# Performance work log

Hardware: AMD Instinct MI355X
Metric: run time of the kernel (lower is better)

Reference implementation:

```python
import jax, jax.numpy as jnp
import numpy as np

B, T, V, D, H, E, K = 512, 80, 80, 128, 256, 8, 2
G1, G2 = 512, 256
EPS = 1e-5


def setup_inputs() -> dict:
    key = jax.random.key(0)
    ks = jax.random.split(key, 16)
    s = 0.05
    x = jax.random.randint(ks[0], (B, T), 0, V)
    emb = jax.random.normal(ks[1], (E, V, D), jnp.float32) * s
    Wih0 = jax.random.normal(ks[2], (E, 4 * H, D), jnp.float32) * s
    Whh0 = jax.random.normal(ks[3], (E, 4 * H, H), jnp.float32) * s
    bih0 = jnp.zeros((E, 4 * H), jnp.float32)
    bhh0 = jnp.zeros((E, 4 * H), jnp.float32)
    Wih1 = jax.random.normal(ks[4], (E, 4 * H, H), jnp.float32) * s
    Whh1 = jax.random.normal(ks[5], (E, 4 * H, H), jnp.float32) * s
    bih1 = jnp.zeros((E, 4 * H), jnp.float32)
    bhh1 = jnp.zeros((E, 4 * H), jnp.float32)
    fcw = jax.random.normal(ks[6], (E, V, H), jnp.float32) * s
    fcb = jnp.zeros((E, V), jnp.float32)
    gw1 = jax.random.normal(ks[7], (G1, D), jnp.float32) * s
    gb1 = jnp.zeros((G1,), jnp.float32)
    bn1_g = jnp.ones((G1,), jnp.float32)
    bn1_b = jnp.zeros((G1,), jnp.float32)
    bn1_m = jnp.zeros((G1,), jnp.float32)
    bn1_v = jnp.ones((G1,), jnp.float32)
    gw2 = jax.random.normal(ks[8], (G2, G1), jnp.float32) * s
    gb2 = jnp.zeros((G2,), jnp.float32)
    bn2_g = jnp.ones((G2,), jnp.float32)
    bn2_b = jnp.zeros((G2,), jnp.float32)
    bn2_m = jnp.zeros((G2,), jnp.float32)
    bn2_v = jnp.ones((G2,), jnp.float32)
    gw3 = jax.random.normal(ks[9], (E, G2), jnp.float32) * s
    gb3 = jnp.zeros((E,), jnp.float32)
    return dict(x=x, emb=emb, Wih0=Wih0, Whh0=Whh0, bih0=bih0, bhh0=bhh0,
                Wih1=Wih1, Whh1=Whh1, bih1=bih1, bhh1=bhh1, fcw=fcw, fcb=fcb,
                gw1=gw1, gb1=gb1, bn1_g=bn1_g, bn1_b=bn1_b, bn1_m=bn1_m, bn1_v=bn1_v,
                gw2=gw2, gb2=gb2, bn2_g=bn2_g, bn2_b=bn2_b, bn2_m=bn2_m, bn2_v=bn2_v,
                gw3=gw3, gb3=gb3)


def _lstm_layer(Wih, Whh, bih, bhh, xs):
    # xs: [B, T, Din] -> (hidden seq [B, T, H], final hidden [B, H]); torch gate order i,f,g,o
    h0 = jnp.zeros((xs.shape[0], Whh.shape[1]), xs.dtype)

    def step(carry, xt):
        h, c = carry
        z = xt @ Wih.T + bih + h @ Whh.T + bhh
        i, f, g, o = jnp.split(z, 4, axis=-1)
        c = jax.nn.sigmoid(f) * c + jax.nn.sigmoid(i) * jnp.tanh(g)
        h = jax.nn.sigmoid(o) * jnp.tanh(c)
        return (h, c), h

    (h, _), hs = jax.lax.scan(step, (h0, h0), jnp.swapaxes(xs, 0, 1))
    return jnp.swapaxes(hs, 0, 1), h


def _expert(emb_e, Wih0, Whh0, bih0, bhh0, Wih1, Whh1, bih1, bhh1, fcw, fcb, x):
    e = emb_e[x]                                   # [B, T, D]
    hs1, _ = _lstm_layer(Wih0, Whh0, bih0, bhh0, e)
    _, h2 = _lstm_layer(Wih1, Whh1, bih1, bhh1, hs1)
    return h2 @ fcw.T + fcb                        # [B, V] (fc on last timestep)


def _bn_eval(x, g, b, m, v):
    return (x - m) * jax.lax.rsqrt(v + EPS) * g + b


def _forward(x, emb, Wih0, Whh0, bih0, bhh0, Wih1, Whh1, bih1, bhh1, fcw, fcb,
             gw1, gb1, bn1_g, bn1_b, bn1_m, bn1_v,
             gw2, gb2, bn2_g, bn2_b, bn2_m, bn2_v, gw3, gb3):
    # gating features: expert 0 embedding, mean over time  [B, D]
    feat = emb[0][x].mean(axis=1)
    h = jax.nn.relu(_bn_eval(feat @ gw1.T + gb1, bn1_g, bn1_b, bn1_m, bn1_v))
    h = jax.nn.relu(_bn_eval(h @ gw2.T + gb2, bn2_g, bn2_b, bn2_m, bn2_v))
    logits = h @ gw3.T + gb3                       # [B, E]  (eval: no noise)
    scores = jax.nn.softmax(logits, axis=-1)
    tv, ti = jax.lax.top_k(scores, K)              # [B, K]
    w = tv / tv.sum(axis=-1, keepdims=True)
    # per-expert combine weight (top-k indices are distinct, at most one slot per expert)
    we = (w[..., None] * jax.nn.one_hot(ti, E, dtype=w.dtype)).sum(axis=1)  # [B, E]
    eouts = jax.vmap(_expert, in_axes=(0,) * 11 + (None,))(
        emb, Wih0, Whh0, bih0, bhh0, Wih1, Whh1, bih1, bhh1, fcw, fcb, x)   # [E, B, V]
    return jnp.einsum('ebc,be->bc', eouts, we)


def reference(x, emb, Wih0, Whh0, bih0, bhh0, Wih1, Whh1, bih1, bhh1, fcw, fcb,
              gw1, gb1, bn1_g, bn1_b, bn1_m, bn1_v,
              gw2, gb2, bn2_g, bn2_b, bn2_m, bn2_v, gw3, gb3):
    return _forward(x, emb, Wih0, Whh0, bih0, bhh0, Wih1, Whh1, bih1, bhh1, fcw, fcb,
                    gw1, gb1, bn1_g, bn1_b, bn1_m, bn1_v,
                    gw2, gb2, bn2_g, bn2_b, bn2_m, bn2_v, gw3, gb3)
```

## Files before the change

kernel.cpp:

```cpp
#include <hip/hip_runtime.h>
#include <hip/hip_bf16.h>
#include <math.h>

#define BB 512
#define TT 80
#define VV 80
#define DD 128
#define HH 256
#define FH 1024
#define EE 8
#define GG1 512
#define GG2 256
#define MT 16
#define NT 72
#define SLOTS (NT*MT)
#define CCK 16

typedef __attribute__((ext_vector_type(8))) short bf16x8;
typedef __attribute__((ext_vector_type(4))) float f32x4;
typedef __attribute__((ext_vector_type(4))) unsigned int u32x4;

__device__ __forceinline__ float bf2f(unsigned short u) {
    unsigned int v = ((unsigned int)u) << 16;
    return __builtin_bit_cast(float, v);
}
__device__ __forceinline__ unsigned short f2bf(float f) {
    __hip_bfloat16 h = __float2bfloat16(f);
    return __builtin_bit_cast(unsigned short, h);
}
__device__ __forceinline__ float sigm(float x) { return 1.f / (1.f + __expf(-x)); }
__device__ __forceinline__ float tanh_f(float x) {
    float ax = fabsf(x);
    float r = 1.f - 2.f / (__expf(2.f * ax) + 1.f);
    return x < 0.f ? -r : r;
}

__global__ void prep_kernel(const float* __restrict__ Whh0, const float* __restrict__ Wih1,
                            const float* __restrict__ Whh1,
                            const float* __restrict__ bih1, const float* __restrict__ bhh1,
                            unsigned short* __restrict__ WR0, unsigned short* __restrict__ WR1,
                            unsigned short* __restrict__ WG, float* __restrict__ bsum1)
{
    const int NB = 262144;
    const int ntot = 3 * NB + EE * FH;
    for (int idx = blockIdx.x * blockDim.x + threadIdx.x; idx < ntot;
         idx += gridDim.x * blockDim.x) {
        if (idx < 3 * NB) {
            int arr = idx / NB;
            int p = idx - arr * NB;
            int gc, kk, e;
            const float* src;
            if (arr < 2) {
                int l = p & 63, nf = (p >> 6) & 7, kb = (p >> 9) & 7, w = (p >> 12) & 7;
                e = (p >> 15) & 7;
                int g = nf >> 1, hc = nf & 1;
                gc = g * 256 + w * 32 + hc * 16 + (l & 15);
                kk = kb * 32 + ((l >> 4) * 8);
                src = (arr == 0) ? Whh0 : Whh1;
            } else {
                int l = p & 63, kb = (p >> 6) & 7, gf = (p >> 9) & 63; e = (p >> 15) & 7;
                gc = gf * 16 + (l & 15);
                kk = kb * 32 + ((l >> 4) * 8);
                src = Wih1;
            }
            const float* sp = src + ((size_t)e * FH + gc) * HH + kk;
            float4 f0 = *(const float4*)sp;
            float4 f1 = *(const float4*)(sp + 4);
            unsigned short out[8];
            out[0] = f2bf(f0.x); out[1] = f2bf(f0.y); out[2] = f2bf(f0.z); out[3] = f2bf(f0.w);
            out[4] = f2bf(f1.x); out[5] = f2bf(f1.y); out[6] = f2bf(f1.z); out[7] = f2bf(f1.w);
            unsigned short* dst = (arr == 0 ? WR0 : arr == 1 ? WR1 : WG) + (size_t)p * 8;
            *(uint4*)dst = *(uint4*)out;
        } else {
            int p = idx - 3 * NB;
            bsum1[p] = bih1[p] + bhh1[p];
        }
    }
}

__global__ __launch_bounds__(256)
void embw_kernel(const float* __restrict__ emb, const float* __restrict__ Wih0,
                 const float* __restrict__ bih0, const float* __restrict__ bhh0,
                 unsigned short* __restrict__ embT)
{
    const int e = blockIdx.x, g = blockIdx.y;
    const int tid = threadIdx.x;
    const int gc = g * 256 + tid;
    __shared__ float er[DD * VV];
    for (int i = tid; i < VV * DD; i += 256) {
        int tok = i >> 7, d = i & 127;
        er[d * VV + tok] = emb[((size_t)e * VV + tok) * DD + d];
    }
    __syncthreads();
    float acc[VV];
    #pragma unroll
    for (int v = 0; v < VV; v++) acc[v] = 0.f;
    const float* wr = Wih0 + ((size_t)e * FH + gc) * DD;
    for (int d = 0; d < DD; d++) {
        float wv = wr[d];
        #pragma unroll
        for (int v4 = 0; v4 < VV; v4 += 4) {
            float4 ev = *(const float4*)&er[d * VV + v4];
            acc[v4] += ev.x * wv; acc[v4 + 1] += ev.y * wv;
            acc[v4 + 2] += ev.z * wv; acc[v4 + 3] += ev.w * wv;
        }
    }
    float bias = bih0[e * FH + gc] + bhh0[e * FH + gc];
    #pragma unroll 4
    for (int v = 0; v < VV; v++)
        embT[(((size_t)e * VV + v) * 256 + tid) * 4 + g] = f2bf(acc[v] + bias);
}

__global__ __launch_bounds__(128)
void gating_kernel(const int* __restrict__ x, const float* __restrict__ emb,
                   const float* __restrict__ gw1, const float* __restrict__ gb1,
                   const float* __restrict__ g1g, const float* __restrict__ g1b,
                   const float* __restrict__ g1m, const float* __restrict__ g1v,
                   const float* __restrict__ gw2, const float* __restrict__ gb2,
                   const float* __restrict__ g2g, const float* __restrict__ g2b,
                   const float* __restrict__ g2m, const float* __restrict__ g2v,
                   const float* __restrict__ gw3, const float* __restrict__ gb3,
                   int* __restrict__ route_i, float* __restrict__ route_w)
{
    int b = blockIdx.x, tid = threadIdx.x;
    __shared__ int tk[TT];
    __shared__ float feat[DD];
    __shared__ float h1[GG1];
    __shared__ float h2[GG2];
    __shared__ float lg[EE];
    if (tid < TT) tk[tid] = x[b * TT + tid];
    __syncthreads();
    if (tid < DD) {
        float s = 0.f;
        for (int t = 0; t < TT; t++) s += emb[(size_t)tk[t] * DD + tid];
        feat[tid] = s * (1.f / TT);
    }
    __syncthreads();
    for (int j = tid; j < GG1; j += 128) {
        float s = gb1[j];
        const float* wr = gw1 + (size_t)j * DD;
        for (int d = 0; d < DD; d++) s += feat[d] * wr[d];
        float y = (s - g1m[j]) / sqrtf(g1v[j] + 1e-5f) * g1g[j] + g1b[j];
        h1[j] = y > 0.f ? y : 0.f;
    }
    __syncthreads();
    for (int j = tid; j < GG2; j += 128) {
        float s = gb2[j];
        const float* wr = gw2 + (size_t)j * GG1;
        for (int d = 0; d < GG1; d++) s += h1[d] * wr[d];
        float y = (s - g2m[j]) / sqrtf(g2v[j] + 1e-5f) * g2g[j] + g2b[j];
        h2[j] = y > 0.f ? y : 0.f;
    }
    __syncthreads();
    if (tid < EE) {
        float s = gb3[tid];
        const float* wr = gw3 + (size_t)tid * GG2;
        for (int d = 0; d < GG2; d++) s += h2[d] * wr[d];
        lg[tid] = s;
    }
    __syncthreads();
    if (tid == 0) {
        int i0 = 0;
        for (int i = 1; i < EE; i++) if (lg[i] > lg[i0]) i0 = i;
        int i1 = (i0 == 0) ? 1 : 0;
        for (int i = 0; i < EE; i++) if (i != i0 && lg[i] > lg[i1]) i1 = i;
        float e1 = expf(lg[i1] - lg[i0]);
        float inv = 1.f / (1.f + e1);
        route_i[b * 2] = i0; route_i[b * 2 + 1] = i1;
        route_w[b * 2] = inv; route_w[b * 2 + 1] = e1 * inv;
    }
}

__global__ __launch_bounds__(1024)
void route_kernel(const int* __restrict__ route_i, const float* __restrict__ route_w,
                  int* __restrict__ slot_b, int* __restrict__ slot_k,
                  float* __restrict__ slot_w, int* __restrict__ slot_e)
{
    __shared__ int wcnt[16][EE];
    __shared__ int cnt[EE];
    __shared__ int off[EE + 1];
    int tid = threadIdx.x;
    int lane = tid & 63, wv = tid >> 6;
    int e = route_i[tid];
    unsigned long long below = (1ull << lane) - 1ull;
    int rankw = 0;
    #pragma unroll
    for (int q = 0; q < EE; q++) {
        unsigned long long m = __ballot(e == q);
        if (q == e) rankw = __popcll(m & below);
        if (lane == 0) wcnt[wv][q] = __popcll(m);
    }
    __syncthreads();
    if (tid < EE) {
        int c = 0;
        for (int w2 = 0; w2 < 16; w2++) c += wcnt[w2][tid];
        cnt[tid] = c;
    }
    __syncthreads();
    if (tid == 0) {
        off[0] = 0;
        for (int q = 0; q < EE; q++) off[q + 1] = off[q] + ((cnt[q] + MT - 1) / MT) * MT;
    }
    __syncthreads();
    for (int s = tid; s < SLOTS; s += 1024) {
        int e2 = 0;
        if (s < off[EE]) { for (int q = 0; q < EE; q++) if (s >= off[q]) e2 = q; }
        slot_b[s] = -1; slot_k[s] = 0; slot_w[s] = 0.f; slot_e[s] = e2;
    }
    __syncthreads();
    int rank = rankw;
    for (int w2 = 0; w2 < wv; w2++) rank += wcnt[w2][e];
    int s = off[e] + rank;
    slot_b[s] = tid >> 1; slot_k[s] = tid & 1; slot_w[s] = route_w[tid];
}

template<int LAYER>
__device__ __forceinline__ void lstm_body(
    int t0, int tcount,
    const unsigned short* __restrict__ WR,
    const unsigned short* __restrict__ embT,
    const unsigned short* __restrict__ zin1,
    const int* __restrict__ x,
    const int* __restrict__ slot_b, const int* __restrict__ slot_e,
    unsigned short* __restrict__ h0seq, float* __restrict__ h1f,
    float* __restrict__ cst, unsigned short* __restrict__ hsv,
    unsigned short (*wlds)[8][8][512], unsigned short (*hbuf)[4096], int* toks)
{
    const int tile = blockIdx.x;
    if (slot_b[tile * MT] < 0) return;
    const int tid = threadIdx.x;
    const int lane = tid & 63;
    const int w = tid >> 6;
    const int e = slot_e[tile * MT];
    const int l15 = lane & 15;
    const int q = lane >> 4;
    const int col0 = w * 32 + l15;
    const int col1 = col0 + 16;
    const int sc0 = (((col0 >> 5) * 64 + 16 * ((col0 >> 3) & 3)) << 3) + (col0 & 7);
    const int sc1 = (((col1 >> 5) * 64 + 16 * ((col1 >> 3) & 3)) << 3) + (col1 & 7);

    const unsigned short* WBg = WR + ((size_t)(e * 8 + w) * 64) * 512 + (size_t)lane * 8;

    u32x4 wres[32];
    #pragma unroll
    for (int i = 0; i < 32; i++) wres[i] = *(const u32x4*)(WBg + (size_t)i * 512);
    #pragma unroll
    for (int i = 0; i < 32; i++) asm volatile("" : "+v"(wres[i]));

    #pragma unroll
    for (int i = 0; i < 16; i++)
        *(uint4*)&wlds[i >> 3][w][i & 7][lane * 8] = *(const uint4*)(WBg + (size_t)(32 + i) * 512);

    if (LAYER == 0) {
        for (int i = tid; i < tcount * 16; i += 512)
            toks[i] = x[max(slot_b[tile * MT + (i & 15)], 0) * TT + t0 + (i >> 4)];
    }

    if (t0 == 0) {
        *(f32x4*)&hbuf[0][tid * 8] = (f32x4){0.f, 0.f, 0.f, 0.f};
    } else {
        *(bf16x8*)&hbuf[0][tid * 8] = *(const bf16x8*)(hsv + (size_t)tile * 4096 + tid * 8);
    }
    float c[8];
    if (t0 == 0) {
        #pragma unroll
        for (int i = 0; i < 8; i++) c[i] = 0.f;
    } else {
        f32x4 v0 = *(const f32x4*)&cst[((size_t)(tile * 512 + tid)) * 8];
        f32x4 v1 = *(const f32x4*)&cst[((size_t)(tile * 512 + tid)) * 8 + 4];
        c[0]=v0[0]; c[1]=v0[1]; c[2]=v0[2]; c[3]=v0[3];
        c[4]=v1[0]; c[5]=v1[1]; c[6]=v1[2]; c[7]=v1[3];
    }

    __syncthreads();

    int cur = 0;
    for (int t = 0; t < tcount; t++) {
        const int nxt = cur ^ 1;

        u32x4 ws[8];
        #pragma unroll
        for (int nf = 0; nf < 8; nf++) ws[nf] = *(const u32x4*)(WBg + (size_t)(48 + nf) * 512);

        ushort4 za[4], zb[4];
        if (LAYER == 0) {
            #pragma unroll
            for (int reg = 0; reg < 4; reg++) {
                int tok = toks[t * 16 + q * 4 + reg];
                const unsigned short* zp = embT + ((size_t)(e * VV + tok)) * 1024;
                za[reg] = *(const ushort4*)(zp + col0 * 4);
                zb[reg] = *(const ushort4*)(zp + col1 * 4);
            }
        } else {
            const unsigned short* zp = zin1 + ((size_t)(tile * tcount + t)) * 16384;
            #pragma unroll
            for (int g = 0; g < 4; g++) {
                int gfa = g * 16 + w * 2;
                za[g] = *(const ushort4*)(zp + (gfa * 64 + lane) * 4);
                zb[g] = *(const ushort4*)(zp + ((gfa + 1) * 64 + lane) * 4);
            }
        }

        f32x4 acc[8];
        if (LAYER == 0) {
            #pragma unroll
            for (int reg = 0; reg < 4; reg++) {
                acc[0][reg] = bf2f(za[reg].x); acc[2][reg] = bf2f(za[reg].y);
                acc[4][reg] = bf2f(za[reg].z); acc[6][reg] = bf2f(za[reg].w);
                acc[1][reg] = bf2f(zb[reg].x); acc[3][reg] = bf2f(zb[reg].y);
                acc[5][reg] = bf2f(zb[reg].z); acc[7][reg] = bf2f(zb[reg].w);
            }
        } else {
            #pragma unroll
            for (int g = 0; g < 4; g++) {
                acc[g * 2][0] = bf2f(za[g].x); acc[g * 2][1] = bf2f(za[g].y);
                acc[g * 2][2] = bf2f(za[g].z); acc[g * 2][3] = bf2f(za[g].w);
                acc[g * 2 + 1][0] = bf2f(zb[g].x); acc[g * 2 + 1][1] = bf2f(zb[g].y);
                acc[g * 2 + 1][2] = bf2f(zb[g].z); acc[g * 2 + 1][3] = bf2f(zb[g].w);
            }
        }

        #pragma unroll
        for (int kb = 0; kb < 4; kb++) {
            bf16x8 a = *(const bf16x8*)&hbuf[cur][(kb * 64 + lane) * 8];
            #pragma unroll
            for (int nf = 0; nf < 8; nf++)
                acc[nf] = __builtin_amdgcn_mfma_f32_16x16x32_bf16(
                    a, __builtin_bit_cast(bf16x8, wres[kb * 8 + nf]), acc[nf], 0, 0, 0);
        }

        #pragma unroll
        for (int kbi = 0; kbi < 2; kbi++) {
            bf16x8 a = *(const bf16x8*)&hbuf[cur][((4 + kbi) * 64 + lane) * 8];
            #pragma unroll
            for (int nf = 0; nf < 8; nf++) {
                bf16x8 wl = *(const bf16x8*)&wlds[kbi][w][nf][lane * 8];
                acc[nf] = __builtin_amdgcn_mfma_f32_16x16x32_bf16(a, wl, acc[nf], 0, 0, 0);
            }
        }

        {
            bf16x8 a = *(const bf16x8*)&hbuf[cur][(6 * 64 + lane) * 8];
            #pragma unroll
            for (int nf = 0; nf < 8; nf++)
                acc[nf] = __builtin_amdgcn_mfma_f32_16x16x32_bf16(
                    a, __builtin_bit_cast(bf16x8, ws[nf]), acc[nf], 0, 0, 0);
        }
        #pragma unroll
        for (int nf = 0; nf < 8; nf++) ws[nf] = *(const u32x4*)(WBg + (size_t)(56 + nf) * 512);
        {
            bf16x8 a = *(const bf16x8*)&hbuf[cur][(7 * 64 + lane) * 8];
            #pragma unroll
            for (int nf = 0; nf < 8; nf++)
                acc[nf] = __builtin_amdgcn_mfma_f32_16x16x32_bf16(
                    a, __builtin_bit_cast(bf16x8, ws[nf]), acc[nf], 0, 0, 0);
        }

        #pragma unroll
        for (int reg = 0; reg < 4; reg++) {
            int r = q * 4 + reg;
            {
                float iv = acc[0][reg], fv = acc[2][reg], gv = acc[4][reg], ov = acc[6][reg];
                float cn = sigm(fv) * c[reg * 2] + sigm(iv) * tanh_f(gv);
                float hn = sigm(ov) * tanh_f(cn);
                c[reg * 2] = cn;
                hbuf[nxt][sc0 + r * 8] = f2bf(hn);
                if (LAYER == 1 && t0 + t == TT - 1)
                    h1f[((size_t)(tile * MT + r)) * HH + col0] = hn;
            }
            {
                float iv = acc[1][reg], fv = acc[3][reg], gv = acc[5][reg], ov = acc[7][reg];
                float cn = sigm(fv) * c[reg * 2 + 1] + sigm(iv) * tanh_f(gv);
                float hn = sigm(ov) * tanh_f(cn);
                c[reg * 2 + 1] = cn;
                hbuf[nxt][sc1 + r * 8] = f2bf(hn);
                if (LAYER == 1 && t0 + t == TT - 1)
                    h1f[((size_t)(tile * MT + r)) * HH + col1] = hn;
            }
        }
        __syncthreads();
        cur = nxt;
        if (LAYER == 0) {
            *(uint4*)(h0seq + ((size_t)(tile * tcount + t)) * 4096 + tid * 8) =
                *(const uint4*)&hbuf[cur][tid * 8];
        }
    }

    f32x4 v0, v1;
    v0[0]=c[0]; v0[1]=c[1]; v0[2]=c[2]; v0[3]=c[3];
    v1[0]=c[4]; v1[1]=c[5]; v1[2]=c[6]; v1[3]=c[7];
    *(f32x4*)&cst[((size_t)(tile * 512 + tid)) * 8] = v0;
    *(f32x4*)&cst[((size_t)(tile * 512 + tid)) * 8 + 4] = v1;
    *(uint4*)(hsv + (size_t)tile * 4096 + tid * 8) = *(const uint4*)&hbuf[cur][tid * 8];
}

__global__ __launch_bounds__(512, 1)
void lstm_fused(int t0_0, int t0_1, int tcount,
                const unsigned short* __restrict__ WR0, const unsigned short* __restrict__ WR1,
                const unsigned short* __restrict__ embT, const unsigned short* __restrict__ zin1,
                const int* __restrict__ x,
                const int* __restrict__ slot_b, const int* __restrict__ slot_e,
                unsigned short* __restrict__ h0seq, float* __restrict__ h1f,
                float* __restrict__ cst0, float* __restrict__ cst1,
                unsigned short* __restrict__ hsv0, unsigned short* __restrict__ hsv1)
{
    __shared__ unsigned short wlds[2][8][8][512];
    __shared__ unsigned short hbuf[2][4096];
    __shared__ int toks[CCK * 16];
    if (blockIdx.y == 0) {
        if (t0_0 < 0) return;
        lstm_body<0>(t0_0, tcount, WR0, embT, zin1, x, slot_b, slot_e,
                     h0seq, h1f, cst0, hsv0, wlds, hbuf, toks);
    } else {
        if (t0_1 < 0) return;
        lstm_body<1>(t0_1, tcount, WR1, embT, zin1, x, slot_b, slot_e,
                     h0seq, h1f, cst1, hsv1, wlds, hbuf, toks);
    }
}

__global__ __launch_bounds__(256)
void gemm_zin(int tcount,
              const unsigned short* __restrict__ h0seq,
              const unsigned short* __restrict__ WG,
              const float* __restrict__ bsum1,
              const int* __restrict__ slot_b, const int* __restrict__ slot_e,
              unsigned short* __restrict__ zin1)
{
    const int tile = blockIdx.x;
    if (slot_b[tile * MT] < 0) return;
    const int tch = blockIdx.y, nch = blockIdx.z;
    const int tid = threadIdx.x, lane = tid & 63, w = tid >> 6;
    const int e = slot_e[tile * MT];
    __shared__ unsigned short Abuf[32768];
    const unsigned short* Asrc = h0seq + ((size_t)(tile * tcount + tch * 8)) * 4096;
    #pragma unroll
    for (int i = 0; i < 16; i++) {
        int o = (i * 256 + tid) * 8;
        *(bf16x8*)&Abuf[o] = *(const bf16x8*)&Asrc[o];
    }
    __syncthreads();
    const unsigned short* Bp = WG + ((size_t)(e * 64 + nch * 16 + w * 4)) * 4096 + lane * 8;
    f32x4 acc[8][4];
    #pragma unroll
    for (int mf = 0; mf < 8; mf++)
        #pragma unroll
        for (int nfi = 0; nfi < 4; nfi++) acc[mf][nfi] = (f32x4){0.f, 0.f, 0.f, 0.f};
    #pragma unroll
    for (int kb = 0; kb < 8; kb++) {
        bf16x8 b0 = *(const bf16x8*)(Bp + 0 * 4096 + kb * 512);
        bf16x8 b1 = *(const bf16x8*)(Bp + 1 * 4096 + kb * 512);
        bf16x8 b2 = *(const bf16x8*)(Bp + 2 * 4096 + kb * 512);
        bf16x8 b3 = *(const bf16x8*)(Bp + 3 * 4096 + kb * 512);
        #pragma unroll
        for (int mf = 0; mf < 8; mf++) {
            bf16x8 a = *(const bf16x8*)&Abuf[(mf * 8 + kb) * 512 + lane * 8];
            acc[mf][0] = __builtin_amdgcn_mfma_f32_16x16x32_bf16(a, b0, acc[mf][0], 0, 0, 0);
            acc[mf][1] = __builtin_amdgcn_mfma_f32_16x16x32_bf16(a, b1, acc[mf][1], 0, 0, 0);
            acc[mf][2] = __builtin_amdgcn_mfma_f32_16x16x32_bf16(a, b2, acc[mf][2], 0, 0, 0);
            acc[mf][3] = __builtin_amdgcn_mfma_f32_16x16x32_bf16(a, b3, acc[mf][3], 0, 0, 0);
        }
    }
    const int l15 = lane & 15;
    #pragma unroll
    for (int mf = 0; mf < 8; mf++) {
        unsigned short* ob = zin1 + ((size_t)(tile * tcount + tch * 8 + mf)) * 16384;
        #pragma unroll
        for (int nfi = 0; nfi < 4; nfi++) {
            int gf = nch * 16 + w * 4 + nfi;
            float bs = bsum1[e * FH + gf * 16 + l15];
            ushort4 v;
            v.x = f2bf(acc[mf][nfi][0] + bs);
            v.y = f2bf(acc[mf][nfi][1] + bs);
            v.z = f2bf(acc[mf][nfi][2] + bs);
            v.w = f2bf(acc[mf][nfi][3] + bs);
            *(ushort4*)(ob + (size_t)(gf * 64 + lane) * 4) = v;
        }
    }
}

__global__ __launch_bounds__(256)
void fc_kernel(const float* __restrict__ fcw, const float* __restrict__ fcb,
               const float* __restrict__ h1f,
               const int* __restrict__ slot_b, const int* __restrict__ slot_k,
               const float* __restrict__ slot_w, const int* __restrict__ slot_e,
               float* __restrict__ wout)
{
    int s = blockIdx.x;
    int b = slot_b[s];
    if (b < 0) return;
    int tid = threadIdx.x;
    __shared__ float hv[HH];
    if (tid < HH) hv[tid] = h1f[(size_t)s * HH + tid];
    __syncthreads();
    int e = slot_e[s], kk = slot_k[s];
    float w = slot_w[s];
    for (int v = tid; v < VV; v += 256) {
        float sacc = fcb[e * VV + v];
        const float* fr = fcw + ((size_t)e * VV + v) * HH;
        #pragma unroll 4
        for (int d = 0; d < HH; d++) sacc += hv[d] * fr[d];
        wout[((size_t)b * 2 + kk) * VV + v] = w * sacc;
    }
}

__global__ void combine_kernel(const float* __restrict__ wout, float* __restrict__ out)
{
    int i = blockIdx.x * blockDim.x + threadIdx.x;
    if (i < BB * VV) {
        int b = i / VV, v = i % VV;
        out[i] = wout[((size_t)b * 2) * VV + v] + wout[((size_t)b * 2 + 1) * VV + v];
    }
}

extern "C" void kernel_launch(void* const* d_in, const int* in_sizes, int n_in,
                              void* d_out, int out_size, void* d_ws, size_t ws_size,
                              hipStream_t stream)
{
    const int*   x    = (const int*)d_in[0];
    const float* emb  = (const float*)d_in[1];
    const float* Wih0 = (const float*)d_in[2];
    const float* Whh0 = (const float*)d_in[3];
    const float* bih0 = (const float*)d_in[4];
    const float* bhh0 = (const float*)d_in[5];
    const float* Wih1 = (const float*)d_in[6];
    const float* Whh1 = (const float*)d_in[7];
    const float* bih1 = (const float*)d_in[8];
    const float* bhh1 = (const float*)d_in[9];
    const float* fcw  = (const float*)d_in[10];
    const float* fcb  = (const float*)d_in[11];
    const float* gw1  = (const float*)d_in[12];
    const float* gb1  = (const float*)d_in[13];
    const float* b1g  = (const float*)d_in[14];
    const float* b1b  = (const float*)d_in[15];
    const float* b1m  = (const float*)d_in[16];
    const float* b1v  = (const float*)d_in[17];
    const float* gw2  = (const float*)d_in[18];
    const float* gb2  = (const float*)d_in[19];
    const float* b2g  = (const float*)d_in[20];
    const float* b2b  = (const float*)d_in[21];
    const float* b2m  = (const float*)d_in[22];
    const float* b2v  = (const float*)d_in[23];
    const float* gw3  = (const float*)d_in[24];
    const float* gb3  = (const float*)d_in[25];

    const size_t NWsh = 262144 * 8;

    char* base = (char*)d_ws;
    size_t o = 0;
    auto alloc = [&](size_t bytes) { char* p = base + o; o = (o + bytes + 255) & ~(size_t)255; return p; };

    unsigned short* WR0  = (unsigned short*)alloc(NWsh * 2);
    unsigned short* WR1  = (unsigned short*)alloc(NWsh * 2);
    unsigned short* WG   = (unsigned short*)alloc(NWsh * 2);
    unsigned short* embT = (unsigned short*)alloc((size_t)EE * VV * FH * 2);
    float* bsum1 = (float*)alloc((size_t)EE * FH * 4);
    float* h1f   = (float*)alloc((size_t)SLOTS * HH * 4);
    float* wout  = (float*)alloc((size_t)BB * 2 * VV * 4);
    float* cst0  = (float*)alloc((size_t)NT * 512 * 8 * 4);
    float* cst1  = (float*)alloc((size_t)NT * 512 * 8 * 4);
    unsigned short* hsv0 = (unsigned short*)alloc((size_t)NT * 4096 * 2);
    unsigned short* hsv1 = (unsigned short*)alloc((size_t)NT * 4096 * 2);
    float* route_w = (float*)alloc((size_t)BB * 2 * 4);
    float* slot_w  = (float*)alloc((size_t)SLOTS * 4);
    int* route_i = (int*)alloc((size_t)BB * 2 * 4);
    int* slot_b  = (int*)alloc((size_t)SLOTS * 4);
    int* slot_k  = (int*)alloc((size_t)SLOTS * 4);
    int* slot_e  = (int*)alloc((size_t)SLOTS * 4);
    unsigned short* h0seq = (unsigned short*)alloc((size_t)NT * CCK * 4096 * 2);
    unsigned short* zin1  = (unsigned short*)alloc((size_t)NT * CCK * 16384 * 2);

    prep_kernel<<<3104, 256, 0, stream>>>(Whh0, Wih1, Whh1, bih1, bhh1, WR0, WR1, WG, bsum1);
    embw_kernel<<<dim3(EE, 4), 256, 0, stream>>>(emb, Wih0, bih0, bhh0, embT);
    gating_kernel<<<BB, 128, 0, stream>>>(x, emb, gw1, gb1, b1g, b1b, b1m, b1v,
                                          gw2, gb2, b2g, b2b, b2m, b2v, gw3, gb3,
                                          route_i, route_w);
    route_kernel<<<1, 1024, 0, stream>>>(route_i, route_w, slot_b, slot_k, slot_w, slot_e);

    const int nch = TT / CCK;
    for (int ph = 0; ph <= nch; ph++) {
        int t00 = (ph < nch) ? ph * CCK : -1;
        int t01 = (ph > 0) ? (ph - 1) * CCK : -1;
        lstm_fused<<<dim3(NT, 2), 512, 0, stream>>>(t00, t01, CCK, WR0, WR1, embT, zin1, x,
                                                    slot_b, slot_e, h0seq, h1f,
                                                    cst0, cst1, hsv0, hsv1);
        if (ph < nch)
            gemm_zin<<<dim3(NT, CCK / 8, 4), 256, 0, stream>>>(CCK, h0seq, WG, bsum1,
                                                               slot_b, slot_e, zin1);
    }

    fc_kernel<<<SLOTS, 256, 0, stream>>>(fcw, fcb, h1f, slot_b, slot_k, slot_w, slot_e, wout);
    combine_kernel<<<(BB * VV + 255) / 256, 256, 0, stream>>>(wout, (float*)d_out);
}
```

Baseline: 836.7 us.

## Fuse input-projection GEMM into LSTM launch as third pipeline stage, prefetch z inputs

The separate gemm_zin launch is removed. Its work now runs as a third blockIdx.y slice of lstm_fused, forming a three-stage software pipeline (layer0 chunk, GEMM on the previous chunk, layer1 on the chunk before that). h0seq and zin are double-buffered so the stages can run in the same launch without conflicts. The per-step input-gate loads are also prefetched one timestep ahead to hide global latency. In exchange the pipeline gains one extra phase, and the GEMM now runs on fewer, larger blocks per tile (72 blocks instead of 576), which may lengthen the critical path.

```diff
diff --git a/kernel.cpp b/kernel.cpp
--- a/kernel.cpp
+++ b/kernel.cpp
@@ -219,7 +219,7 @@
     int t0, int tcount,
     const unsigned short* __restrict__ WR,
     const unsigned short* __restrict__ embT,
-    const unsigned short* __restrict__ zin1,
+    const unsigned short* __restrict__ zin,
     const int* __restrict__ x,
     const int* __restrict__ slot_b, const int* __restrict__ slot_e,
     unsigned short* __restrict__ h0seq, float* __restrict__ h1f,
@@ -274,32 +274,54 @@
 
     __syncthreads();
 
+    ushort4 za[4], zb[4];
+    if (LAYER == 0) {
+        #pragma unroll
+        for (int reg = 0; reg < 4; reg++) {
+            int tok = toks[q * 4 + reg];
+            const unsigned short* zp = embT + ((size_t)(e * VV + tok)) * 1024;
+            za[reg] = *(const ushort4*)(zp + col0 * 4);
+            zb[reg] = *(const ushort4*)(zp + col1 * 4);
+        }
+    } else {
+        const unsigned short* zp = zin + ((size_t)(tile * tcount)) * 16384;
+        #pragma unroll
+        for (int g = 0; g < 4; g++) {
+            int gfa = g * 16 + w * 2;
+            za[g] = *(const ushort4*)(zp + (gfa * 64 + lane) * 4);
+            zb[g] = *(const ushort4*)(zp + ((gfa + 1) * 64 + lane) * 4);
+        }
+    }
+
     int cur = 0;
     for (int t = 0; t < tcount; t++) {
         const int nxt = cur ^ 1;
 
+        ushort4 zan[4], zbn[4];
+        {
+            int tn = (t + 1 < tcount) ? t + 1 : t;
+            if (LAYER == 0) {
+                #pragma unroll
+                for (int reg = 0; reg < 4; reg++) {
+                    int tok = toks[tn * 16 + q * 4 + reg];
+                    const unsigned short* zp = embT + ((size_t)(e * VV + tok)) * 1024;
+                    zan[reg] = *(const ushort4*)(zp + col0 * 4);
+                    zbn[reg] = *(const ushort4*)(zp + col1 * 4);
+                }
+            } else {
+                const unsigned short* zp = zin + ((size_t)(tile * tcount + tn)) * 16384;
+                #pragma unroll
+                for (int g = 0; g < 4; g++) {
+                    int gfa = g * 16 + w * 2;
+                    zan[g] = *(const ushort4*)(zp + (gfa * 64 + lane) * 4);
+                    zbn[g] = *(const ushort4*)(zp + ((gfa + 1) * 64 + lane) * 4);
+                }
+            }
+        }
+
         u32x4 ws[8];
         #pragma unroll
         for (int nf = 0; nf < 8; nf++) ws[nf] = *(const u32x4*)(WBg + (size_t)(48 + nf) * 512);
-
-        ushort4 za[4], zb[4];
-        if (LAYER == 0) {
-            #pragma unroll
-            for (int reg = 0; reg < 4; reg++) {
-                int tok = toks[t * 16 + q * 4 + reg];
-                const unsigned short* zp = embT + ((size_t)(e * VV + tok)) * 1024;
-                za[reg] = *(const ushort4*)(zp + col0 * 4);
-                zb[reg] = *(const ushort4*)(zp + col1 * 4);
-            }
-        } else {
-            const unsigned short* zp = zin1 + ((size_t)(tile * tcount + t)) * 16384;
-            #pragma unroll
-            for (int g = 0; g < 4; g++) {
-                int gfa = g * 16 + w * 2;
-                za[g] = *(const ushort4*)(zp + (gfa * 64 + lane) * 4);
-                zb[g] = *(const ushort4*)(zp + ((gfa + 1) * 64 + lane) * 4);
-            }
-        }
 
         f32x4 acc[8];
         if (LAYER == 0) {
@@ -380,6 +402,8 @@
         }
         __syncthreads();
         cur = nxt;
+        #pragma unroll
+        for (int i = 0; i < 4; i++) { za[i] = zan[i]; zb[i] = zbn[i]; }
         if (LAYER == 0) {
             *(uint4*)(h0seq + ((size_t)(tile * tcount + t)) * 4096 + tid * 8) =
                 *(const uint4*)&hbuf[cur][tid * 8];
@@ -394,13 +418,81 @@
     *(uint4*)(hsv + (size_t)tile * 4096 + tid * 8) = *(const uint4*)&hbuf[cur][tid * 8];
 }
 
+__device__ __forceinline__ void gemm_body(
+    int tcount,
+    const unsigned short* __restrict__ h0seq,
+    const unsigned short* __restrict__ WG,
+    const float* __restrict__ bsum1,
+    const int* __restrict__ slot_b, const int* __restrict__ slot_e,
+    unsigned short* __restrict__ zin1,
+    unsigned short* Abuf)
+{
+    const int tile = blockIdx.x;
+    if (slot_b[tile * MT] < 0) return;
+    const int tid = threadIdx.x, lane = tid & 63, w = tid >> 6;
+    const int e = slot_e[tile * MT];
+    const int l15 = lane & 15;
+    for (int tch = 0; tch < tcount / 8; tch++) {
+        const unsigned short* Asrc = h0seq + ((size_t)(tile * tcount + tch * 8)) * 4096;
+        #pragma unroll
+        for (int i = 0; i < 8; i++) {
+            int o = (i * 512 + tid) * 8;
+            *(bf16x8*)&Abuf[o] = *(const bf16x8*)&Asrc[o];
+        }
+        __syncthreads();
+        #pragma unroll
+        for (int gh = 0; gh < 2; gh++) {
+            const unsigned short* Bp = WG + ((size_t)(e * 64 + w * 8 + gh * 4)) * 4096 + (size_t)lane * 8;
+            f32x4 acc[8][4];
+            #pragma unroll
+            for (int mf = 0; mf < 8; mf++)
+                #pragma unroll
+                for (int nfi = 0; nfi < 4; nfi++) acc[mf][nfi] = (f32x4){0.f, 0.f, 0.f, 0.f};
+            #pragma unroll
+            for (int kb = 0; kb < 8; kb++) {
+                bf16x8 b0 = *(const bf16x8*)(Bp + 0 * 4096 + kb * 512);
+                bf16x8 b1 = *(const bf16x8*)(Bp + 1 * 4096 + kb * 512);
+                bf16x8 b2 = *(const bf16x8*)(Bp + 2 * 4096 + kb * 512);
+                bf16x8 b3 = *(const bf16x8*)(Bp + 3 * 4096 + kb * 512);
+                #pragma unroll
+                for (int mf = 0; mf < 8; mf++) {
+                    bf16x8 a = *(const bf16x8*)&Abuf[(mf * 8 + kb) * 512 + lane * 8];
+                    acc[mf][0] = __builtin_amdgcn_mfma_f32_16x16x32_bf16(a, b0, acc[mf][0], 0, 0, 0);
+                    acc[mf][1] = __builtin_amdgcn_mfma_f32_16x16x32_bf16(a, b1, acc[mf][1], 0, 0, 0);
+                    acc[mf][2] = __builtin_amdgcn_mfma_f32_16x16x32_bf16(a, b2, acc[mf][2], 0, 0, 0);
+                    acc[mf][3] = __builtin_amdgcn_mfma_f32_16x16x32_bf16(a, b3, acc[mf][3], 0, 0, 0);
+                }
+            }
+            #pragma unroll
+            for (int mf = 0; mf < 8; mf++) {
+                unsigned short* ob = zin1 + ((size_t)(tile * tcount + tch * 8 + mf)) * 16384;
+                #pragma unroll
+                for (int nfi = 0; nfi < 4; nfi++) {
+                    int gf = w * 8 + gh * 4 + nfi;
+                    float bs = bsum1[e * FH + gf * 16 + l15];
+                    ushort4 v;
+                    v.x = f2bf(acc[mf][nfi][0] + bs);
+                    v.y = f2bf(acc[mf][nfi][1] + bs);
+                    v.z = f2bf(acc[mf][nfi][2] + bs);
+                    v.w = f2bf(acc[mf][nfi][3] + bs);
+                    *(ushort4*)(ob + (size_t)(gf * 64 + lane) * 4) = v;
+                }
+            }
+        }
+        __syncthreads();
+    }
+}
+
 __global__ __launch_bounds__(512, 1)
-void lstm_fused(int t0_0, int t0_1, int tcount,
+void lstm_fused(int t00, int t01, int tg, int tcount,
                 const unsigned short* __restrict__ WR0, const unsigned short* __restrict__ WR1,
-                const unsigned short* __restrict__ embT, const unsigned short* __restrict__ zin1,
+                const unsigned short* __restrict__ WG, const float* __restrict__ bsum1,
+                const unsigned short* __restrict__ embT,
+                unsigned short* __restrict__ h0_w, const unsigned short* __restrict__ h0_r,
+                unsigned short* __restrict__ zin_w, const unsigned short* __restrict__ zin_r,
                 const int* __restrict__ x,
                 const int* __restrict__ slot_b, const int* __restrict__ slot_e,
-                unsigned short* __restrict__ h0seq, float* __restrict__ h1f,
+                float* __restrict__ h1f,
                 float* __restrict__ cst0, float* __restrict__ cst1,
                 unsigned short* __restrict__ hsv0, unsigned short* __restrict__ hsv1)
 {
@@ -408,73 +500,16 @@
     __shared__ unsigned short hbuf[2][4096];
     __shared__ int toks[CCK * 16];
     if (blockIdx.y == 0) {
-        if (t0_0 < 0) return;
-        lstm_body<0>(t0_0, tcount, WR0, embT, zin1, x, slot_b, slot_e,
-                     h0seq, h1f, cst0, hsv0, wlds, hbuf, toks);
+        if (t00 < 0) return;
+        lstm_body<0>(t00, tcount, WR0, embT, nullptr, x, slot_b, slot_e,
+                     h0_w, h1f, cst0, hsv0, wlds, hbuf, toks);
+    } else if (blockIdx.y == 1) {
+        if (t01 < 0) return;
+        lstm_body<1>(t01, tcount, WR1, embT, zin_r, x, slot_b, slot_e,
+                     nullptr, h1f, cst1, hsv1, wlds, hbuf, toks);
     } else {
-        if (t0_1 < 0) return;
-        lstm_body<1>(t0_1, tcount, WR1, embT, zin1, x, slot_b, slot_e,
-                     h0seq, h1f, cst1, hsv1, wlds, hbuf, toks);
-    }
-}
-
-__global__ __launch_bounds__(256)
-void gemm_zin(int tcount,
-              const unsigned short* __restrict__ h0seq,
-              const unsigned short* __restrict__ WG,
-              const float* __restrict__ bsum1,
-              const int* __restrict__ slot_b, const int* __restrict__ slot_e,
-              unsigned short* __restrict__ zin1)
-{
-    const int tile = blockIdx.x;
-    if (slot_b[tile * MT] < 0) return;
-    const int tch = blockIdx.y, nch = blockIdx.z;
-    const int tid = threadIdx.x, lane = tid & 63, w = tid >> 6;
-    const int e = slot_e[tile * MT];
-    __shared__ unsigned short Abuf[32768];
-    const unsigned short* Asrc = h0seq + ((size_t)(tile * tcount + tch * 8)) * 4096;
-    #pragma unroll
-    for (int i = 0; i < 16; i++) {
-        int o = (i * 256 + tid) * 8;
-        *(bf16x8*)&Abuf[o] = *(const bf16x8*)&Asrc[o];
-    }
-    __syncthreads();
-    const unsigned short* Bp = WG + ((size_t)(e * 64 + nch * 16 + w * 4)) * 4096 + lane * 8;
-    f32x4 acc[8][4];
-    #pragma unroll
-    for (int mf = 0; mf < 8; mf++)
-        #pragma unroll
-        for (int nfi = 0; nfi < 4; nfi++) acc[mf][nfi] = (f32x4){0.f, 0.f, 0.f, 0.f};
-    #pragma unroll
-    for (int kb = 0; kb < 8; kb++) {
-        bf16x8 b0 = *(const bf16x8*)(Bp + 0 * 4096 + kb * 512);
-        bf16x8 b1 = *(const bf16x8*)(Bp + 1 * 4096 + kb * 512);
-        bf16x8 b2 = *(const bf16x8*)(Bp + 2 * 4096 + kb * 512);
-        bf16x8 b3 = *(const bf16x8*)(Bp + 3 * 4096 + kb * 512);
-        #pragma unroll
-        for (int mf = 0; mf < 8; mf++) {
-            bf16x8 a = *(const bf16x8*)&Abuf[(mf * 8 + kb) * 512 + lane * 8];
-            acc[mf][0] = __builtin_amdgcn_mfma_f32_16x16x32_bf16(a, b0, acc[mf][0], 0, 0, 0);
-            acc[mf][1] = __builtin_amdgcn_mfma_f32_16x16x32_bf16(a, b1, acc[mf][1], 0, 0, 0);
-            acc[mf][2] = __builtin_amdgcn_mfma_f32_16x16x32_bf16(a, b2, acc[mf][2], 0, 0, 0);
-            acc[mf][3] = __builtin_amdgcn_mfma_f32_16x16x32_bf16(a, b3, acc[mf][3], 0, 0, 0);
-        }
-    }
-    const int l15 = lane & 15;
-    #pragma unroll
-    for (int mf = 0; mf < 8; mf++) {
-        unsigned short* ob = zin1 + ((size_t)(tile * tcount + tch * 8 + mf)) * 16384;
-        #pragma unroll
-        for (int nfi = 0; nfi < 4; nfi++) {
-            int gf = nch * 16 + w * 4 + nfi;
-            float bs = bsum1[e * FH + gf * 16 + l15];
-            ushort4 v;
-            v.x = f2bf(acc[mf][nfi][0] + bs);
-            v.y = f2bf(acc[mf][nfi][1] + bs);
-            v.z = f2bf(acc[mf][nfi][2] + bs);
-            v.w = f2bf(acc[mf][nfi][3] + bs);
-            *(ushort4*)(ob + (size_t)(gf * 64 + lane) * 4) = v;
-        }
+        if (tg < 0) return;
+        gemm_body(tcount, h0_r, WG, bsum1, slot_b, slot_e, zin_w, &wlds[0][0][0][0]);
     }
 }
 
@@ -566,8 +601,10 @@
     int* slot_b  = (int*)alloc((size_t)SLOTS * 4);
     int* slot_k  = (int*)alloc((size_t)SLOTS * 4);
     int* slot_e  = (int*)alloc((size_t)SLOTS * 4);
-    unsigned short* h0seq = (unsigned short*)alloc((size_t)NT * CCK * 4096 * 2);
-    unsigned short* zin1  = (unsigned short*)alloc((size_t)NT * CCK * 16384 * 2);
+    unsigned short* h0seqA = (unsigned short*)alloc((size_t)NT * CCK * 4096 * 2);
+    unsigned short* h0seqB = (unsigned short*)alloc((size_t)NT * CCK * 4096 * 2);
+    unsigned short* zinA   = (unsigned short*)alloc((size_t)NT * CCK * 16384 * 2);
+    unsigned short* zinB   = (unsigned short*)alloc((size_t)NT * CCK * 16384 * 2);
 
     prep_kernel<<<3104, 256, 0, stream>>>(Whh0, Wih1, Whh1, bih1, bhh1, WR0, WR1, WG, bsum1);
     embw_kernel<<<dim3(EE, 4), 256, 0, stream>>>(emb, Wih0, bih0, bhh0, embT);
@@ -577,15 +614,18 @@
     route_kernel<<<1, 1024, 0, stream>>>(route_i, route_w, slot_b, slot_k, slot_w, slot_e);
 
     const int nch = TT / CCK;
-    for (int ph = 0; ph <= nch; ph++) {
+    for (int ph = 0; ph <= nch + 1; ph++) {
         int t00 = (ph < nch) ? ph * CCK : -1;
-        int t01 = (ph > 0) ? (ph - 1) * CCK : -1;
-        lstm_fused<<<dim3(NT, 2), 512, 0, stream>>>(t00, t01, CCK, WR0, WR1, embT, zin1, x,
-                                                    slot_b, slot_e, h0seq, h1f,
+        int tg  = (ph - 1 >= 0 && ph - 1 < nch) ? (ph - 1) * CCK : -1;
+        int t01 = (ph - 2 >= 0 && ph - 2 < nch) ? (ph - 2) * CCK : -1;
+        unsigned short* h0_w = (ph & 1) ? h0seqB : h0seqA;
+        unsigned short* h0_r = ((ph - 1) & 1) ? h0seqB : h0seqA;
+        unsigned short* zn_w = ((ph - 1) & 1) ? zinB : zinA;
+        unsigned short* zn_r = ((ph - 2) & 1) ? zinB : zinA;
+        lstm_fused<<<dim3(NT, 3), 512, 0, stream>>>(t00, t01, tg, CCK, WR0, WR1, WG, bsum1,
+                                                    embT, h0_w, h0_r, zn_w, zn_r, x,
+                                                    slot_b, slot_e, h1f,
                                                     cst0, cst1, hsv0, hsv1);
-        if (ph < nch)
-            gemm_zin<<<dim3(NT, CCK / 8, 4), 256, 0, stream>>>(CCK, h0seq, WG, bsum1,
-                                                               slot_b, slot_e, zin1);
     }
 
     fc_kernel<<<SLOTS, 256, 0, stream>>>(fcw, fcb, h1f, slot_b, slot_k, slot_w, slot_e, wout);
```

Result: faster. 775.4 us (median of 2 runs) (-7.3%).
